# Performance work log

Hardware: AMD Instinct MI355X
Metric: run time of the kernel (lower is better)

## Reference

```python
import jax, jax.numpy as jnp
import numpy as np

HIDDEN = 1024
HEADS = 16
HEAD_DIM = HIDDEN // HEADS  # 64
BLOCK = 1024  # block_size; seq_len > BLOCK triggers ring path
B, S = 1, 4096


def setup_inputs() -> dict:
    key = jax.random.key(0)
    k0, k1, k2, k3, k4 = jax.random.split(key, 5)
    w_scale = 0.02
    return {
        "hidden_states": jax.random.normal(k0, (B, S, HIDDEN), dtype=jnp.float32),
        # weights stored [in, out]; applied as x @ W (equivalent to nn.Linear with W.T)
        "w_q": jax.random.normal(k1, (HIDDEN, HIDDEN), dtype=jnp.float32) * w_scale,
        "w_k": jax.random.normal(k2, (HIDDEN, HIDDEN), dtype=jnp.float32) * w_scale,
        "w_v": jax.random.normal(k3, (HIDDEN, HIDDEN), dtype=jnp.float32) * w_scale,
        "w_o": jax.random.normal(k4, (HIDDEN, HIDDEN), dtype=jnp.float32) * w_scale,
    }


def _ring_attention(q, k, v, block, scale):
    # q,k,v: [B, H, S, D]. Faithful to the torch module: each KV block subtracts
    # its OWN local max (no running-max rescale); exp-sums and weighted-V are
    # accumulated additively across KV blocks, then normalized once at the end.
    b, h, s, d = q.shape
    nb = s // block
    kb = jnp.moveaxis(k.reshape(b, h, nb, block, d), 2, 0)  # [nb, B, H, block, D]
    vb = jnp.moveaxis(v.reshape(b, h, nb, block, d), 2, 0)

    def step(carry, kv):
        num, den = carry
        k_blk, v_blk = kv
        s_blk = jnp.einsum("bhqd,bhkd->bhqk", q, k_blk) * scale  # [B,H,S,block]
        m = jnp.max(s_blk, axis=-1, keepdims=True)               # local max only
        e = jnp.exp(s_blk - m)
        num = num + jnp.einsum("bhqk,bhkd->bhqd", e, v_blk)
        den = den + jnp.sum(e, axis=-1, keepdims=True)
        return (num, den), None

    init = (jnp.zeros_like(q), jnp.zeros((b, h, s, 1), dtype=q.dtype))
    (num, den), _ = jax.lax.scan(step, init, (kb, vb))
    return num / den


def reference(hidden_states, w_q, w_k, w_v, w_o):
    b, s, _ = hidden_states.shape
    q = (hidden_states @ w_q).reshape(b, s, HEADS, HEAD_DIM).transpose(0, 2, 1, 3)
    k = (hidden_states @ w_k).reshape(b, s, HEADS, HEAD_DIM).transpose(0, 2, 1, 3)
    v = (hidden_states @ w_v).reshape(b, s, HEADS, HEAD_DIM).transpose(0, 2, 1, 3)
    scale = HEAD_DIM ** -0.5
    out = _ring_attention(q, k, v, BLOCK, scale)          # [B,H,S,D]
    out = out.transpose(0, 2, 1, 3).reshape(b, s, HIDDEN)  # [B,S,hidden]
    return out @ w_o
```

## Files before the change

kernel.cpp:

```cpp
#include <hip/hip_runtime.h>
#include <hip/hip_bf16.h>

typedef __bf16 bf16;
typedef bf16 bf16x2 __attribute__((ext_vector_type(2)));
typedef bf16 bf16x4 __attribute__((ext_vector_type(4)));
typedef bf16 bf16x8 __attribute__((ext_vector_type(8)));
typedef float f32x4 __attribute__((ext_vector_type(4)));

#define HID 1024
#define NHEADS 16
#define HD 64
#define SEQ 4096

__device__ __forceinline__ void gll16(const void* g, void* l) {
  __builtin_amdgcn_global_load_lds(
      (const __attribute__((address_space(1))) void*)g,
      (__attribute__((address_space(3))) void*)l, 16, 0, 0);
}

__device__ __forceinline__ float fast_exp2(float x) {
#if __has_builtin(__builtin_amdgcn_exp2f)
  return __builtin_amdgcn_exp2f(x);
#else
  return __expf(x * 0.6931471805599453f);
#endif
}

__global__ __launch_bounds__(256)
void prep_kernel(const float* __restrict__ X,
                 const float* __restrict__ Wq, const float* __restrict__ Wk,
                 const float* __restrict__ Wv, const float* __restrict__ Wo,
                 bf16* __restrict__ Xb, bf16* __restrict__ Wt)
{
  const int z = blockIdx.z, t = threadIdx.x, bx = blockIdx.x;
  if (z == 0) {
    const float4* src = (const float4*)X;
    const int gid = bx * 256 + t;
    #pragma unroll
    for (int i = 0; i < 16; ++i) {
      float4 v = src[gid + i * 65536];
      bf16x4 o = {(bf16)v.x, (bf16)v.y, (bf16)v.z, (bf16)v.w};
      *(bf16x4*)&Xb[(size_t)(gid + i * 65536) * 4] = o;
    }
  } else {
    const float* W = (z == 1) ? Wq : (z == 2) ? Wk : (z == 3) ? Wv : Wo;
    bf16* dst = Wt + (size_t)(z - 1) * HID * HID;
    const float scale = (z == 1) ? 0.18033688011112042f : 1.0f;
    __shared__ bf16 T[64][68];
    const int tr = (bx >> 4) * 64, tc = (bx & 15) * 64;
    #pragma unroll
    for (int p = 0; p < 4; ++p) {
      int row = (t >> 4) + p * 16;
      float4 v = *(const float4*)&W[(size_t)(tr + row) * HID + tc + (t & 15) * 4];
      T[row][(t & 15) * 4 + 0] = (bf16)(v.x * scale);
      T[row][(t & 15) * 4 + 1] = (bf16)(v.y * scale);
      T[row][(t & 15) * 4 + 2] = (bf16)(v.z * scale);
      T[row][(t & 15) * 4 + 3] = (bf16)(v.w * scale);
    }
    __syncthreads();
    #pragma unroll
    for (int p = 0; p < 4; ++p) {
      int rp = (t >> 4) + p * 16;
      int cb = (t & 15) * 4;
      bf16x4 o = {T[cb + 0][rp], T[cb + 1][rp], T[cb + 2][rp], T[cb + 3][rp]};
      *(bf16x4*)&dst[(size_t)(tc + rp) * HID + tr + cb] = o;
    }
  }
}

__global__ __launch_bounds__(256)
void qkv_gemm(const bf16* __restrict__ A, const bf16* __restrict__ Wt,
              bf16* __restrict__ Qg, bf16* __restrict__ Kg,
              bf16* __restrict__ Vt)
{
  __shared__ bf16 sbuf[16384];
  bf16* As = sbuf;
  bf16* Bs = sbuf + 8192;

  const int t = threadIdx.x, lane = t & 63, w = t >> 6;
  const int z = blockIdx.z;
  const int n0 = blockIdx.x * 128, m0 = blockIdx.y * 128;
  const bf16* Bt = Wt + (size_t)z * HID * HID;
  const int wm = (w & 1) * 64, wn = (w >> 1) * 64;
  const int fr = lane & 15, quad = lane >> 4;

  f32x4 acc[4][4] = {};

  const int sr = lane >> 3;
  const int sc = ((lane & 7) - sr) & 7;
  const bf16* ga = A  + (size_t)(m0 + w * 32 + sr) * HID + sc * 8;
  const bf16* gb = Bt + (size_t)(n0 + w * 32 + sr) * HID + sc * 8;

  for (int k0 = 0; k0 < HID; k0 += 64) {
    __syncthreads();
    #pragma unroll
    for (int c = 0; c < 4; ++c) {
      gll16(ga + (size_t)(c * 8) * HID + k0, As + (w * 32 + c * 8) * 64);
      gll16(gb + (size_t)(c * 8) * HID + k0, Bs + (w * 32 + c * 8) * 64);
    }
    __syncthreads();
    #pragma unroll
    for (int ks = 0; ks < 2; ++ks) {
      bf16x8 af[4], bg[4];
      #pragma unroll
      for (int i = 0; i < 4; ++i)
        af[i] = *(const bf16x8*)&As[(wm + i * 16 + fr) * 64 +
                                    ((ks * 4 + quad + fr) & 7) * 8];
      #pragma unroll
      for (int i = 0; i < 4; ++i)
        bg[i] = *(const bf16x8*)&Bs[(wn + i * 16 + fr) * 64 +
                                    ((ks * 4 + quad + fr) & 7) * 8];
      #pragma unroll
      for (int mi = 0; mi < 4; ++mi)
        #pragma unroll
        for (int ni = 0; ni < 4; ++ni)
          acc[mi][ni] = __builtin_amdgcn_mfma_f32_16x16x32_bf16(
              af[mi], bg[ni], acc[mi][ni], 0, 0, 0);
    }
  }

  if (z < 2) {
    bf16* C = z ? Kg : Qg;
    #pragma unroll
    for (int mi = 0; mi < 4; ++mi)
      #pragma unroll
      for (int ni = 0; ni < 4; ++ni)
        #pragma unroll
        for (int r = 0; r < 4; ++r)
          C[(size_t)(m0 + wm + mi * 16 + quad * 4 + r) * HID +
            n0 + wn + ni * 16 + fr] = (bf16)acc[mi][ni][r];
  } else {
    __syncthreads();
    #pragma unroll
    for (int mi = 0; mi < 4; ++mi)
      #pragma unroll
      for (int ni = 0; ni < 4; ++ni)
        #pragma unroll
        for (int r = 0; r < 4; ++r) {
          int row = wn + ni * 16 + fr;
          int col = wm + mi * 16 + quad * 4 + r;
          int colS = (col + 8 * (row & 15)) & 127;
          sbuf[row * 128 + colS] = (bf16)acc[mi][ni][r];
        }
    __syncthreads();
    const int row = t >> 1, cb = (t & 1) * 64;
    #pragma unroll
    for (int j = 0; j < 8; ++j) {
      int c0 = (cb + j * 8 + 8 * (row & 15)) & 127;
      *(bf16x8*)&Vt[(size_t)(n0 + row) * SEQ + m0 + cb + j * 8] =
          *(const bf16x8*)&sbuf[row * 128 + c0];
    }
  }
}

__global__ __launch_bounds__(256)
void oproj_gemm(const bf16* __restrict__ A, const bf16* __restrict__ Bt,
                float* __restrict__ C)
{
  __shared__ bf16 sbuf[16384];
  bf16* As = sbuf;
  bf16* Bs = sbuf + 8192;

  const int t = threadIdx.x, lane = t & 63, w = t >> 6;
  const int n0 = blockIdx.x * 128, m0 = blockIdx.y * 128;
  const int wm = (w & 1) * 64, wn = (w >> 1) * 64;
  const int fr = lane & 15, quad = lane >> 4;

  f32x4 acc[4][4] = {};

  const int sr = lane >> 3;
  const int sc = ((lane & 7) - sr) & 7;
  const bf16* ga = A  + (size_t)(m0 + w * 32 + sr) * HID + sc * 8;
  const bf16* gb = Bt + (size_t)(n0 + w * 32 + sr) * HID + sc * 8;

  for (int k0 = 0; k0 < HID; k0 += 64) {
    __syncthreads();
    #pragma unroll
    for (int c = 0; c < 4; ++c) {
      gll16(ga + (size_t)(c * 8) * HID + k0, As + (w * 32 + c * 8) * 64);
      gll16(gb + (size_t)(c * 8) * HID + k0, Bs + (w * 32 + c * 8) * 64);
    }
    __syncthreads();
    #pragma unroll
    for (int ks = 0; ks < 2; ++ks) {
      bf16x8 af[4], bg[4];
      #pragma unroll
      for (int i = 0; i < 4; ++i)
        af[i] = *(const bf16x8*)&As[(wm + i * 16 + fr) * 64 +
                                    ((ks * 4 + quad + fr) & 7) * 8];
      #pragma unroll
      for (int i = 0; i < 4; ++i)
        bg[i] = *(const bf16x8*)&Bs[(wn + i * 16 + fr) * 64 +
                                    ((ks * 4 + quad + fr) & 7) * 8];
      #pragma unroll
      for (int mi = 0; mi < 4; ++mi)
        #pragma unroll
        for (int ni = 0; ni < 4; ++ni)
          acc[mi][ni] = __builtin_amdgcn_mfma_f32_16x16x32_bf16(
              af[mi], bg[ni], acc[mi][ni], 0, 0, 0);
    }
  }

  #pragma unroll
  for (int mi = 0; mi < 4; ++mi)
    #pragma unroll
    for (int ni = 0; ni < 4; ++ni)
      #pragma unroll
      for (int r = 0; r < 4; ++r)
        C[(size_t)(m0 + wm + mi * 16 + quad * 4 + r) * HID +
          n0 + wn + ni * 16 + fr] = acc[mi][ni][r];
}

#define THR_L2 12.0f

__global__ __launch_bounds__(256, 2)
void attn5(const bf16* __restrict__ Q, const bf16* __restrict__ K,
           const bf16* __restrict__ Vt, bf16* __restrict__ O)
{
  __shared__ bf16 Ks[2][4096];
  __shared__ bf16 Vs[2][4096];
  __shared__ bf16 Ps[4][1024];

  const int t = threadIdx.x, lane = t & 63, w = t >> 6;
  const int h = blockIdx.y, q0 = blockIdx.x * 128;
  const int fr = lane & 15, quad = lane >> 4;

  bf16x8 bq[2][2];
  #pragma unroll
  for (int qf = 0; qf < 2; ++qf)
    #pragma unroll
    for (int ks = 0; ks < 2; ++ks)
      bq[qf][ks] = *(const bf16x8*)&Q[(size_t)(q0 + w * 32 + qf * 16 + fr) * HID
                                      + h * 64 + ks * 32 + quad * 8];

  const int sr = lane >> 3;
  const int sc = ((lane & 7) - sr) & 7;
  const bf16* gk = K  + (size_t)(w * 16 + sr) * HID + h * 64 + sc * 8;
  const bf16* gv = Vt + (size_t)(h * 64 + w * 16 + sr) * SEQ + sc * 8;

  #pragma unroll
  for (int j = 0; j < 2; ++j) {
    gll16(gk + (size_t)(j * 8) * HID, &Ks[0][(w * 16 + j * 8) * 64]);
    gll16(gv + (size_t)(j * 8) * SEQ, &Vs[0][(w * 16 + j * 8) * 64]);
  }

  f32x4 accN[2][4] = {};
  f32x4 accO[2][4] = {};
  float m_used[2] = {-3e38f, -3e38f}, m_true[2] = {-3e38f, -3e38f};
  float l_i[2] = {0.f, 0.f}, den[2] = {0.f, 0.f};

  __syncthreads();

  for (int kk = 0; kk < 64; ++kk) {
    const int buf = kk & 1;
    if (kk < 63) {
      const size_t key0n = (size_t)(kk + 1) * 64;
      #pragma unroll
      for (int j = 0; j < 2; ++j) {
        gll16(gk + (key0n + j * 8) * HID, &Ks[buf ^ 1][(w * 16 + j * 8) * 64]);
        gll16(gv + key0n + (size_t)(j * 8) * SEQ,
              &Vs[buf ^ 1][(w * 16 + j * 8) * 64]);
      }
    }

    bf16x8 ak[4][2];
    #pragma unroll
    for (int mt = 0; mt < 4; ++mt)
      #pragma unroll
      for (int ks = 0; ks < 2; ++ks)
        ak[mt][ks] = *(const bf16x8*)&Ks[buf][(mt * 16 + fr) * 64 +
                                             ((ks * 4 + quad + fr) & 7) * 8];

    f32x4 s[2][4];
    #pragma unroll
    for (int qf = 0; qf < 2; ++qf)
      #pragma unroll
      for (int mt = 0; mt < 4; ++mt) {
        f32x4 z = {};
        z = __builtin_amdgcn_mfma_f32_16x16x32_bf16(ak[mt][0], bq[qf][0], z, 0, 0, 0);
        z = __builtin_amdgcn_mfma_f32_16x16x32_bf16(ak[mt][1], bq[qf][1], z, 0, 0, 0);
        s[qf][mt] = z;
      }

    bf16x8 bp[2][2];
    #pragma unroll
    for (int qf = 0; qf < 2; ++qf) {
      float mx0 = fmaxf(fmaxf(s[qf][0][0], s[qf][0][1]), fmaxf(s[qf][0][2], s[qf][0][3]));
      float mx1 = fmaxf(fmaxf(s[qf][1][0], s[qf][1][1]), fmaxf(s[qf][1][2], s[qf][1][3]));
      float mx2 = fmaxf(fmaxf(s[qf][2][0], s[qf][2][1]), fmaxf(s[qf][2][2], s[qf][2][3]));
      float mx3 = fmaxf(fmaxf(s[qf][3][0], s[qf][3][1]), fmaxf(s[qf][3][2], s[qf][3][3]));
      float mx = fmaxf(fmaxf(mx0, mx1), fmaxf(mx2, mx3));
      mx = fmaxf(mx, __shfl_xor(mx, 16));
      mx = fmaxf(mx, __shfl_xor(mx, 32));
      m_true[qf] = fmaxf(m_true[qf], mx);

      if (__any(mx > m_used[qf] + THR_L2)) {
        const float mn = fmaxf(m_used[qf], mx);
        const float a = fast_exp2(m_used[qf] - mn);
        m_used[qf] = mn;
        l_i[qf] *= a;
        #pragma unroll
        for (int dt = 0; dt < 4; ++dt) accO[qf][dt] *= a;
      }

      float sum = 0.f;
      const int prow = fr * 64;
      #pragma unroll
      for (int mt = 0; mt < 4; ++mt) {
        float p0 = fast_exp2(s[qf][mt][0] - m_used[qf]);
        float p1 = fast_exp2(s[qf][mt][1] - m_used[qf]);
        float p2 = fast_exp2(s[qf][mt][2] - m_used[qf]);
        float p3 = fast_exp2(s[qf][mt][3] - m_used[qf]);
        sum += (p0 + p1) + (p2 + p3);
        bf16x4 pv = {(bf16)p0, (bf16)p1, (bf16)p2, (bf16)p3};
        *(bf16x4*)&Ps[w][prow + ((mt * 2 + (quad >> 1) + fr) & 7) * 8 +
                         (quad & 1) * 4] = pv;
      }
      sum += __shfl_xor(sum, 16);
      sum += __shfl_xor(sum, 32);
      l_i[qf] += sum;

      #pragma unroll
      for (int ks = 0; ks < 2; ++ks)
        bp[qf][ks] = *(const bf16x8*)&Ps[w][fr * 64 +
                                            ((ks * 4 + quad + fr) & 7) * 8];
    }

    #pragma unroll
    for (int ks = 0; ks < 2; ++ks)
      #pragma unroll
      for (int dt = 0; dt < 4; ++dt) {
        bf16x8 av = *(const bf16x8*)&Vs[buf][(dt * 16 + fr) * 64 +
                                            ((ks * 4 + quad + fr) & 7) * 8];
        accO[0][dt] = __builtin_amdgcn_mfma_f32_16x16x32_bf16(av, bp[0][ks], accO[0][dt], 0, 0, 0);
        accO[1][dt] = __builtin_amdgcn_mfma_f32_16x16x32_bf16(av, bp[1][ks], accO[1][dt], 0, 0, 0);
      }

    if ((kk & 15) == 15) {
      #pragma unroll
      for (int qf = 0; qf < 2; ++qf) {
        const float c = fast_exp2(m_used[qf] - m_true[qf]);
        den[qf] += l_i[qf] * c;
        #pragma unroll
        for (int dt = 0; dt < 4; ++dt)
          #pragma unroll
          for (int r = 0; r < 4; ++r) accN[qf][dt][r] += accO[qf][dt][r] * c;
        #pragma unroll
        for (int dt = 0; dt < 4; ++dt) accO[qf][dt] = (f32x4){0.f, 0.f, 0.f, 0.f};
        l_i[qf] = 0.f; m_used[qf] = -3e38f; m_true[qf] = -3e38f;
      }
    }
    __syncthreads();
  }

  #pragma unroll
  for (int qf = 0; qf < 2; ++qf) {
    const float inv = 1.0f / den[qf];
    const size_t orow = (size_t)(q0 + w * 32 + qf * 16 + fr) * HID + h * 64;
    #pragma unroll
    for (int dt = 0; dt < 4; ++dt) {
      bf16x4 ov = {(bf16)(accN[qf][dt][0] * inv), (bf16)(accN[qf][dt][1] * inv),
                   (bf16)(accN[qf][dt][2] * inv), (bf16)(accN[qf][dt][3] * inv)};
      *(bf16x4*)&O[orow + dt * 16 + quad * 4] = ov;
    }
  }
}

extern "C" void kernel_launch(void* const* d_in, const int* in_sizes, int n_in,
                              void* d_out, int out_size, void* d_ws, size_t ws_size,
                              hipStream_t stream)
{
  const float* X  = (const float*)d_in[0];
  const float* Wq = (const float*)d_in[1];
  const float* Wk = (const float*)d_in[2];
  const float* Wv = (const float*)d_in[3];
  const float* Wo = (const float*)d_in[4];
  float* out = (float*)d_out;

  const size_t MB = 1024 * 1024;
  bf16* Xb  = (bf16*)d_ws;
  bf16* Wt  = (bf16*)((char*)d_ws + 8  * MB);
  bf16* Qg  = (bf16*)((char*)d_ws + 16 * MB);
  bf16* Kg  = (bf16*)((char*)d_ws + 24 * MB);
  bf16* Vtg = (bf16*)((char*)d_ws + 32 * MB);
  bf16* Og  = (bf16*)((char*)d_ws + 40 * MB);

  prep_kernel<<<dim3(256, 1, 5), 256, 0, stream>>>(X, Wq, Wk, Wv, Wo, Xb, Wt);
  qkv_gemm<<<dim3(HID / 128, SEQ / 128, 3), 256, 0, stream>>>(Xb, Wt, Qg, Kg, Vtg);
  attn5<<<dim3(SEQ / 128, NHEADS), 256, 0, stream>>>(Qg, Kg, Vtg, Og);
  oproj_gemm<<<dim3(HID / 128, SEQ / 128), 256, 0, stream>>>(
      Og, Wt + (size_t)3 * HID * HID, out);
}
```

Baseline: 263.2 us.

## Split attention KV range across two blocks and combine partials in separate kernel

The attention kernel now splits the KV sequence into two halves along a new grid dimension, doubling the block count from 512 to 1024, and raises occupancy hints to 4 blocks per CU. Each half writes unnormalized fp32 numerators and denominators to workspace, and a new combine kernel sums them and normalizes into bf16. This targets under-filled CUs on the attention pass. The cost is an extra kernel launch and about 32 MB of fp32 partial traffic, and the fallback path is taken only if the workspace is too small.

```diff
diff --git a/kernel.cpp b/kernel.cpp
--- a/kernel.cpp
+++ b/kernel.cpp
@@ -213,16 +213,17 @@
 
 #define THR_L2 12.0f
 
-__global__ __launch_bounds__(256, 2)
-void attn5(const bf16* __restrict__ Q, const bf16* __restrict__ K,
-           const bf16* __restrict__ Vt, bf16* __restrict__ O)
+__global__ __launch_bounds__(256, 4)
+void attn6(const bf16* __restrict__ Q, const bf16* __restrict__ K,
+           const bf16* __restrict__ Vt, float* __restrict__ Num,
+           float* __restrict__ Den)
 {
   __shared__ bf16 Ks[2][4096];
   __shared__ bf16 Vs[2][4096];
   __shared__ bf16 Ps[4][1024];
 
   const int t = threadIdx.x, lane = t & 63, w = t >> 6;
-  const int h = blockIdx.y, q0 = blockIdx.x * 128;
+  const int h = blockIdx.y, q0 = blockIdx.x * 128, half = blockIdx.z;
   const int fr = lane & 15, quad = lane >> 4;
 
   bf16x8 bq[2][2];
@@ -235,8 +236,8 @@
 
   const int sr = lane >> 3;
   const int sc = ((lane & 7) - sr) & 7;
-  const bf16* gk = K  + (size_t)(w * 16 + sr) * HID + h * 64 + sc * 8;
-  const bf16* gv = Vt + (size_t)(h * 64 + w * 16 + sr) * SEQ + sc * 8;
+  const bf16* gk = K  + (size_t)(half * 2048 + w * 16 + sr) * HID + h * 64 + sc * 8;
+  const bf16* gv = Vt + (size_t)(h * 64 + w * 16 + sr) * SEQ + half * 2048 + sc * 8;
 
   #pragma unroll
   for (int j = 0; j < 2; ++j) {
@@ -251,9 +252,9 @@
 
   __syncthreads();
 
-  for (int kk = 0; kk < 64; ++kk) {
+  for (int kk = 0; kk < 32; ++kk) {
     const int buf = kk & 1;
-    if (kk < 63) {
+    if (kk < 31) {
       const size_t key0n = (size_t)(kk + 1) * 64;
       #pragma unroll
       for (int j = 0; j < 2; ++j) {
@@ -353,6 +354,176 @@
     __syncthreads();
   }
 
+  float* numH = Num + (size_t)half * SEQ * HID;
+  #pragma unroll
+  for (int qf = 0; qf < 2; ++qf) {
+    const int qrow = q0 + w * 32 + qf * 16 + fr;
+    const size_t orow = (size_t)qrow * HID + h * 64;
+    #pragma unroll
+    for (int dt = 0; dt < 4; ++dt)
+      *(f32x4*)&numH[orow + dt * 16 + quad * 4] = accN[qf][dt];
+    if (quad == 0)
+      Den[((size_t)half * 16 + h) * SEQ + qrow] = den[qf];
+  }
+}
+
+__global__ __launch_bounds__(256)
+void combine_kernel(const float* __restrict__ Num, const float* __restrict__ Den,
+                    bf16* __restrict__ Og)
+{
+  const int gid = blockIdx.x * 256 + threadIdx.x;
+  const int idx = gid * 4;
+  const int row = idx >> 10, col = idx & 1023, h = col >> 6;
+  const float d0 = Den[(size_t)h * SEQ + row];
+  const float d1 = Den[((size_t)16 + h) * SEQ + row];
+  const float inv = 1.0f / (d0 + d1);
+  f32x4 a = *(const f32x4*)&Num[idx];
+  f32x4 b = *(const f32x4*)&Num[(size_t)SEQ * HID + idx];
+  bf16x4 o = {(bf16)((a[0] + b[0]) * inv), (bf16)((a[1] + b[1]) * inv),
+              (bf16)((a[2] + b[2]) * inv), (bf16)((a[3] + b[3]) * inv)};
+  *(bf16x4*)&Og[idx] = o;
+}
+
+__global__ __launch_bounds__(256, 2)
+void attn5(const bf16* __restrict__ Q, const bf16* __restrict__ K,
+           const bf16* __restrict__ Vt, bf16* __restrict__ O)
+{
+  __shared__ bf16 Ks[2][4096];
+  __shared__ bf16 Vs[2][4096];
+  __shared__ bf16 Ps[4][1024];
+
+  const int t = threadIdx.x, lane = t & 63, w = t >> 6;
+  const int h = blockIdx.y, q0 = blockIdx.x * 128;
+  const int fr = lane & 15, quad = lane >> 4;
+
+  bf16x8 bq[2][2];
+  #pragma unroll
+  for (int qf = 0; qf < 2; ++qf)
+    #pragma unroll
+    for (int ks = 0; ks < 2; ++ks)
+      bq[qf][ks] = *(const bf16x8*)&Q[(size_t)(q0 + w * 32 + qf * 16 + fr) * HID
+                                      + h * 64 + ks * 32 + quad * 8];
+
+  const int sr = lane >> 3;
+  const int sc = ((lane & 7) - sr) & 7;
+  const bf16* gk = K  + (size_t)(w * 16 + sr) * HID + h * 64 + sc * 8;
+  const bf16* gv = Vt + (size_t)(h * 64 + w * 16 + sr) * SEQ + sc * 8;
+
+  #pragma unroll
+  for (int j = 0; j < 2; ++j) {
+    gll16(gk + (size_t)(j * 8) * HID, &Ks[0][(w * 16 + j * 8) * 64]);
+    gll16(gv + (size_t)(j * 8) * SEQ, &Vs[0][(w * 16 + j * 8) * 64]);
+  }
+
+  f32x4 accN[2][4] = {};
+  f32x4 accO[2][4] = {};
+  float m_used[2] = {-3e38f, -3e38f}, m_true[2] = {-3e38f, -3e38f};
+  float l_i[2] = {0.f, 0.f}, den[2] = {0.f, 0.f};
+
+  __syncthreads();
+
+  for (int kk = 0; kk < 64; ++kk) {
+    const int buf = kk & 1;
+    if (kk < 63) {
+      const size_t key0n = (size_t)(kk + 1) * 64;
+      #pragma unroll
+      for (int j = 0; j < 2; ++j) {
+        gll16(gk + (key0n + j * 8) * HID, &Ks[buf ^ 1][(w * 16 + j * 8) * 64]);
+        gll16(gv + key0n + (size_t)(j * 8) * SEQ,
+              &Vs[buf ^ 1][(w * 16 + j * 8) * 64]);
+      }
+    }
+
+    bf16x8 ak[4][2];
+    #pragma unroll
+    for (int mt = 0; mt < 4; ++mt)
+      #pragma unroll
+      for (int ks = 0; ks < 2; ++ks)
+        ak[mt][ks] = *(const bf16x8*)&Ks[buf][(mt * 16 + fr) * 64 +
+                                             ((ks * 4 + quad + fr) & 7) * 8];
+
+    f32x4 s[2][4];
+    #pragma unroll
+    for (int qf = 0; qf < 2; ++qf)
+      #pragma unroll
+      for (int mt = 0; mt < 4; ++mt) {
+        f32x4 z = {};
+        z = __builtin_amdgcn_mfma_f32_16x16x32_bf16(ak[mt][0], bq[qf][0], z, 0, 0, 0);
+        z = __builtin_amdgcn_mfma_f32_16x16x32_bf16(ak[mt][1], bq[qf][1], z, 0, 0, 0);
+        s[qf][mt] = z;
+      }
+
+    bf16x8 bp[2][2];
+    #pragma unroll
+    for (int qf = 0; qf < 2; ++qf) {
+      float mx0 = fmaxf(fmaxf(s[qf][0][0], s[qf][0][1]), fmaxf(s[qf][0][2], s[qf][0][3]));
+      float mx1 = fmaxf(fmaxf(s[qf][1][0], s[qf][1][1]), fmaxf(s[qf][1][2], s[qf][1][3]));
+      float mx2 = fmaxf(fmaxf(s[qf][2][0], s[qf][2][1]), fmaxf(s[qf][2][2], s[qf][2][3]));
+      float mx3 = fmaxf(fmaxf(s[qf][3][0], s[qf][3][1]), fmaxf(s[qf][3][2], s[qf][3][3]));
+      float mx = fmaxf(fmaxf(mx0, mx1), fmaxf(mx2, mx3));
+      mx = fmaxf(mx, __shfl_xor(mx, 16));
+      mx = fmaxf(mx, __shfl_xor(mx, 32));
+      m_true[qf] = fmaxf(m_true[qf], mx);
+
+      if (__any(mx > m_used[qf] + THR_L2)) {
+        const float mn = fmaxf(m_used[qf], mx);
+        const float a = fast_exp2(m_used[qf] - mn);
+        m_used[qf] = mn;
+        l_i[qf] *= a;
+        #pragma unroll
+        for (int dt = 0; dt < 4; ++dt) accO[qf][dt] *= a;
+      }
+
+      float sum = 0.f;
+      const int prow = fr * 64;
+      #pragma unroll
+      for (int mt = 0; mt < 4; ++mt) {
+        float p0 = fast_exp2(s[qf][mt][0] - m_used[qf]);
+        float p1 = fast_exp2(s[qf][mt][1] - m_used[qf]);
+        float p2 = fast_exp2(s[qf][mt][2] - m_used[qf]);
+        float p3 = fast_exp2(s[qf][mt][3] - m_used[qf]);
+        sum += (p0 + p1) + (p2 + p3);
+        bf16x4 pv = {(bf16)p0, (bf16)p1, (bf16)p2, (bf16)p3};
+        *(bf16x4*)&Ps[w][prow + ((mt * 2 + (quad >> 1) + fr) & 7) * 8 +
+                         (quad & 1) * 4] = pv;
+      }
+      sum += __shfl_xor(sum, 16);
+      sum += __shfl_xor(sum, 32);
+      l_i[qf] += sum;
+
+      #pragma unroll
+      for (int ks = 0; ks < 2; ++ks)
+        bp[qf][ks] = *(const bf16x8*)&Ps[w][fr * 64 +
+                                            ((ks * 4 + quad + fr) & 7) * 8];
+    }
+
+    #pragma unroll
+    for (int ks = 0; ks < 2; ++ks)
+      #pragma unroll
+      for (int dt = 0; dt < 4; ++dt) {
+        bf16x8 av = *(const bf16x8*)&Vs[buf][(dt * 16 + fr) * 64 +
+                                            ((ks * 4 + quad + fr) & 7) * 8];
+        accO[0][dt] = __builtin_amdgcn_mfma_f32_16x16x32_bf16(av, bp[0][ks], accO[0][dt], 0, 0, 0);
+        accO[1][dt] = __builtin_amdgcn_mfma_f32_16x16x32_bf16(av, bp[1][ks], accO[1][dt], 0, 0, 0);
+      }
+
+    if ((kk & 15) == 15) {
+      #pragma unroll
+      for (int qf = 0; qf < 2; ++qf) {
+        const float c = fast_exp2(m_used[qf] - m_true[qf]);
+        den[qf] += l_i[qf] * c;
+        #pragma unroll
+        for (int dt = 0; dt < 4; ++dt)
+          #pragma unroll
+          for (int r = 0; r < 4; ++r) accN[qf][dt][r] += accO[qf][dt][r] * c;
+        #pragma unroll
+        for (int dt = 0; dt < 4; ++dt) accO[qf][dt] = (f32x4){0.f, 0.f, 0.f, 0.f};
+        l_i[qf] = 0.f; m_used[qf] = -3e38f; m_true[qf] = -3e38f;
+      }
+    }
+    __syncthreads();
+  }
+
   #pragma unroll
   for (int qf = 0; qf < 2; ++qf) {
     const float inv = 1.0f / den[qf];
@@ -378,16 +549,23 @@
   float* out = (float*)d_out;
 
   const size_t MB = 1024 * 1024;
-  bf16* Xb  = (bf16*)d_ws;
-  bf16* Wt  = (bf16*)((char*)d_ws + 8  * MB);
-  bf16* Qg  = (bf16*)((char*)d_ws + 16 * MB);
-  bf16* Kg  = (bf16*)((char*)d_ws + 24 * MB);
-  bf16* Vtg = (bf16*)((char*)d_ws + 32 * MB);
-  bf16* Og  = (bf16*)((char*)d_ws + 40 * MB);
+  bf16*  Xb  = (bf16*)d_ws;
+  bf16*  Wt  = (bf16*)((char*)d_ws + 8  * MB);
+  bf16*  Qg  = (bf16*)((char*)d_ws + 16 * MB);
+  bf16*  Kg  = (bf16*)((char*)d_ws + 24 * MB);
+  bf16*  Vtg = (bf16*)((char*)d_ws + 32 * MB);
+  bf16*  Og  = (bf16*)((char*)d_ws + 40 * MB);
+  float* Num = (float*)((char*)d_ws + 48 * MB);
+  float* Den = (float*)((char*)d_ws + 80 * MB);
 
   prep_kernel<<<dim3(256, 1, 5), 256, 0, stream>>>(X, Wq, Wk, Wv, Wo, Xb, Wt);
   qkv_gemm<<<dim3(HID / 128, SEQ / 128, 3), 256, 0, stream>>>(Xb, Wt, Qg, Kg, Vtg);
-  attn5<<<dim3(SEQ / 128, NHEADS), 256, 0, stream>>>(Qg, Kg, Vtg, Og);
+  if (ws_size >= 81 * MB) {
+    attn6<<<dim3(SEQ / 128, NHEADS, 2), 256, 0, stream>>>(Qg, Kg, Vtg, Num, Den);
+    combine_kernel<<<dim3(SEQ * HID / 1024, 1, 1), 256, 0, stream>>>(Num, Den, Og);
+  } else {
+    attn5<<<dim3(SEQ / 128, NHEADS), 256, 0, stream>>>(Qg, Kg, Vtg, Og);
+  }
   oproj_gemm<<<dim3(HID / 128, SEQ / 128), 256, 0, stream>>>(
       Og, Wt + (size_t)3 * HID * HID, out);
 }
```

New measurement: 268.3 us. Within noise of the previous version (+2.0%).

## Split attention KV range across two blocks with 32x32 MFMA and combine kernel

Applied to the files above, without the earlier changes.

Adds attn8, which splits the 4096-key range into two halves via blockIdx.z, doubling the grid and raising occupancy to 4 blocks per CU. Each 32-query wave computes S with 32x32x16 MFMAs and keeps P in registers via cross-lane shuffles, removing the LDS staging of P. It writes normalized per-ring-block partial outputs plus adjusted denominators for each 1024-key block. A new combine8 kernel reweights and sums them into Og. This costs an extra launch and partial-output traffic, and it runs only when the workspace holds at least 81 MB.

```diff
diff --git a/kernel.cpp b/kernel.cpp
--- a/kernel.cpp
+++ b/kernel.cpp
@@ -6,6 +6,8 @@
 typedef bf16 bf16x4 __attribute__((ext_vector_type(4)));
 typedef bf16 bf16x8 __attribute__((ext_vector_type(8)));
 typedef float f32x4 __attribute__((ext_vector_type(4)));
+typedef float f32x16 __attribute__((ext_vector_type(16)));
+typedef unsigned int u32x4 __attribute__((ext_vector_type(4)));
 
 #define HID 1024
 #define NHEADS 16
@@ -212,6 +214,187 @@
 }
 
 #define THR_L2 12.0f
+
+__global__ __launch_bounds__(256, 4)
+void attn8(const bf16* __restrict__ Q, const bf16* __restrict__ K,
+           const bf16* __restrict__ Vt, bf16* __restrict__ Opart,
+           float* __restrict__ Den)
+{
+  __shared__ bf16 Ks[2][4096];
+  __shared__ bf16 Vs[2][4096];
+
+  const int t = threadIdx.x, lane = t & 63, w = t >> 6;
+  const int h = blockIdx.y, q0 = blockIdx.x * 128, half = blockIdx.z;
+  const int q = lane & 31, hi = lane >> 5;
+  const int qrow = q0 + w * 32 + q;
+
+  bf16x8 bq[4];
+  #pragma unroll
+  for (int j = 0; j < 4; ++j)
+    bq[j] = *(const bf16x8*)&Q[(size_t)qrow * HID + h * 64 + j * 16 + hi * 8];
+
+  const int sr = lane >> 3;
+  const int sc = ((lane & 7) - sr) & 7;
+  const bf16* gk = K  + (size_t)(half * 2048 + w * 16 + sr) * HID + h * 64 + sc * 8;
+  const bf16* gv = Vt + (size_t)(h * 64 + w * 16 + sr) * SEQ + half * 2048 + sc * 8;
+
+  #pragma unroll
+  for (int j = 0; j < 2; ++j) {
+    gll16(gk + (size_t)(j * 8) * HID, &Ks[0][(w * 16 + j * 8) * 64]);
+    gll16(gv + (size_t)(j * 8) * SEQ, &Vs[0][(w * 16 + j * 8) * 64]);
+  }
+
+  f32x16 accO[2];
+  #pragma unroll
+  for (int r = 0; r < 16; ++r) { accO[0][r] = 0.f; accO[1][r] = 0.f; }
+  float m_used = -3e38f, m_true = -3e38f, l_i = 0.f;
+
+  __syncthreads();
+
+  for (int kk = 0; kk < 32; ++kk) {
+    const int buf = kk & 1;
+    if (kk < 31) {
+      const size_t key0n = (size_t)(kk + 1) * 64;
+      #pragma unroll
+      for (int j = 0; j < 2; ++j) {
+        gll16(gk + (key0n + j * 8) * HID, &Ks[buf ^ 1][(w * 16 + j * 8) * 64]);
+        gll16(gv + key0n + (size_t)(j * 8) * SEQ,
+              &Vs[buf ^ 1][(w * 16 + j * 8) * 64]);
+      }
+    }
+
+    #pragma unroll
+    for (int st = 0; st < 2; ++st) {
+      const int r0 = st * 32;
+      f32x16 s;
+      #pragma unroll
+      for (int r = 0; r < 16; ++r) s[r] = 0.f;
+      #pragma unroll
+      for (int j = 0; j < 4; ++j) {
+        const int row = r0 + q;
+        bf16x8 ak = *(const bf16x8*)&Ks[buf][row * 64 +
+                                            ((j * 2 + hi + row) & 7) * 8];
+        s = __builtin_amdgcn_mfma_f32_32x32x16_bf16(ak, bq[j], s, 0, 0, 0);
+      }
+
+      float mx = s[0];
+      #pragma unroll
+      for (int r = 1; r < 16; ++r) mx = fmaxf(mx, s[r]);
+      mx = fmaxf(mx, __shfl_xor(mx, 32));
+      m_true = fmaxf(m_true, mx);
+
+      if (__any(mx > m_used + THR_L2)) {
+        const float mn = fmaxf(m_used, mx);
+        const float a = fast_exp2(m_used - mn);
+        m_used = mn; l_i *= a;
+        #pragma unroll
+        for (int r = 0; r < 16; ++r) { accO[0][r] *= a; accO[1][r] *= a; }
+      }
+
+      float p[16], sum = 0.f;
+      #pragma unroll
+      for (int r = 0; r < 16; ++r) { p[r] = fast_exp2(s[r] - m_used); sum += p[r]; }
+      sum += __shfl_xor(sum, 32);
+      l_i += sum;
+
+      unsigned pk[8];
+      #pragma unroll
+      for (int i = 0; i < 8; ++i) {
+        bf16x2 pp = {(bf16)p[2 * i], (bf16)p[2 * i + 1]};
+        pk[i] = __builtin_bit_cast(unsigned, pp);
+      }
+      unsigned e0 = __shfl_xor(hi ? pk[0] : pk[2], 32);
+      unsigned e1 = __shfl_xor(hi ? pk[1] : pk[3], 32);
+      unsigned e2 = __shfl_xor(hi ? pk[4] : pk[6], 32);
+      unsigned e3 = __shfl_xor(hi ? pk[5] : pk[7], 32);
+      u32x4 w0 = {hi ? e0 : pk[0], hi ? e1 : pk[1],
+                  hi ? pk[2] : e0, hi ? pk[3] : e1};
+      u32x4 w1 = {hi ? e2 : pk[4], hi ? e3 : pk[5],
+                  hi ? pk[6] : e2, hi ? pk[7] : e3};
+      bf16x8 bp0 = __builtin_bit_cast(bf16x8, w0);
+      bf16x8 bp1 = __builtin_bit_cast(bf16x8, w1);
+
+      #pragma unroll
+      for (int db = 0; db < 2; ++db) {
+        const int rowd = db * 32 + q;
+        bf16x8 av0 = *(const bf16x8*)&Vs[buf][rowd * 64 +
+                       ((st * 4 + 0 + hi + rowd) & 7) * 8];
+        accO[db] = __builtin_amdgcn_mfma_f32_32x32x16_bf16(av0, bp0, accO[db], 0, 0, 0);
+        bf16x8 av1 = *(const bf16x8*)&Vs[buf][rowd * 64 +
+                       ((st * 4 + 2 + hi + rowd) & 7) * 8];
+        accO[db] = __builtin_amdgcn_mfma_f32_32x32x16_bf16(av1, bp1, accO[db], 0, 0, 0);
+      }
+    }
+
+    if ((kk & 15) == 15) {
+      const int rb = half * 2 + (kk >> 4);
+      const float inv = 1.0f / l_i;
+      const size_t base =
+          ((size_t)(rb * 16 + h) * 128 + (q0 >> 5) + w) * 2048 + (size_t)lane * 32;
+      #pragma unroll
+      for (int j = 0; j < 4; ++j) {
+        bf16x8 wv;
+        #pragma unroll
+        for (int e = 0; e < 8; ++e)
+          wv[e] = (bf16)(accO[j >> 1][(j & 1) * 8 + e] * inv);
+        *(bf16x8*)&Opart[base + j * 8] = wv;
+      }
+      if (hi == 0)
+        Den[(size_t)(rb * 16 + h) * SEQ + qrow] =
+            l_i * fast_exp2(m_used - m_true);
+      #pragma unroll
+      for (int r = 0; r < 16; ++r) { accO[0][r] = 0.f; accO[1][r] = 0.f; }
+      l_i = 0.f; m_used = -3e38f; m_true = -3e38f;
+    }
+    __syncthreads();
+  }
+}
+
+__global__ __launch_bounds__(64)
+void combine8(const bf16* __restrict__ Opart, const float* __restrict__ Den,
+              bf16* __restrict__ Og)
+{
+  __shared__ bf16 T[32][72];
+  const int lane = threadIdx.x & 63;
+  const int h = blockIdx.y, qs = blockIdx.x;
+  const int q = lane & 31, hi = lane >> 5;
+
+  float dw[4];
+  #pragma unroll
+  for (int rb = 0; rb < 4; ++rb)
+    dw[rb] = Den[(size_t)(rb * 16 + h) * SEQ + qs * 32 + q];
+  const float inv = 1.0f / (dw[0] + dw[1] + dw[2] + dw[3]);
+
+  float acc[32];
+  #pragma unroll
+  for (int i = 0; i < 32; ++i) acc[i] = 0.f;
+  #pragma unroll
+  for (int rb = 0; rb < 4; ++rb) {
+    const float wq = dw[rb] * inv;
+    const size_t base =
+        ((size_t)(rb * 16 + h) * 128 + qs) * 2048 + (size_t)lane * 32;
+    #pragma unroll
+    for (int j = 0; j < 4; ++j) {
+      bf16x8 v = *(const bf16x8*)&Opart[base + j * 8];
+      #pragma unroll
+      for (int e = 0; e < 8; ++e) acc[j * 8 + e] += wq * (float)v[e];
+    }
+  }
+
+  #pragma unroll
+  for (int idx = 0; idx < 32; ++idx) {
+    const int db = idx >> 4, r = idx & 15;
+    const int d = db * 32 + (r & 3) + 8 * (r >> 2) + 4 * hi;
+    T[q][d] = (bf16)acc[idx];
+  }
+  __syncthreads();
+  #pragma unroll
+  for (int p = 0; p < 4; ++p) {
+    const int row = p * 8 + (lane >> 3);
+    *(bf16x8*)&Og[(size_t)(qs * 32 + row) * HID + h * 64 + (lane & 7) * 8] =
+        *(const bf16x8*)&T[row][(lane & 7) * 8];
+  }
+}
 
 __global__ __launch_bounds__(256, 2)
 void attn5(const bf16* __restrict__ Q, const bf16* __restrict__ K,
@@ -378,16 +561,23 @@
   float* out = (float*)d_out;
 
   const size_t MB = 1024 * 1024;
-  bf16* Xb  = (bf16*)d_ws;
-  bf16* Wt  = (bf16*)((char*)d_ws + 8  * MB);
-  bf16* Qg  = (bf16*)((char*)d_ws + 16 * MB);
-  bf16* Kg  = (bf16*)((char*)d_ws + 24 * MB);
-  bf16* Vtg = (bf16*)((char*)d_ws + 32 * MB);
-  bf16* Og  = (bf16*)((char*)d_ws + 40 * MB);
+  bf16*  Xb  = (bf16*)d_ws;
+  bf16*  Wt  = (bf16*)((char*)d_ws + 8  * MB);
+  bf16*  Qg  = (bf16*)((char*)d_ws + 16 * MB);
+  bf16*  Kg  = (bf16*)((char*)d_ws + 24 * MB);
+  bf16*  Vtg = (bf16*)((char*)d_ws + 32 * MB);
+  bf16*  Og  = (bf16*)((char*)d_ws + 40 * MB);
+  bf16*  Opart = (bf16*)((char*)d_ws + 48 * MB);
+  float* Den   = (float*)((char*)d_ws + 80 * MB);
 
   prep_kernel<<<dim3(256, 1, 5), 256, 0, stream>>>(X, Wq, Wk, Wv, Wo, Xb, Wt);
   qkv_gemm<<<dim3(HID / 128, SEQ / 128, 3), 256, 0, stream>>>(Xb, Wt, Qg, Kg, Vtg);
-  attn5<<<dim3(SEQ / 128, NHEADS), 256, 0, stream>>>(Qg, Kg, Vtg, Og);
+  if (ws_size >= 81 * MB) {
+    attn8<<<dim3(SEQ / 128, NHEADS, 2), 256, 0, stream>>>(Qg, Kg, Vtg, Opart, Den);
+    combine8<<<dim3(SEQ / 32, NHEADS), 64, 0, stream>>>(Opart, Den, Og);
+  } else {
+    attn5<<<dim3(SEQ / 128, NHEADS), 256, 0, stream>>>(Qg, Kg, Vtg, Og);
+  }
   oproj_gemm<<<dim3(HID / 128, SEQ / 128), 256, 0, stream>>>(
       Og, Wt + (size_t)3 * HID * HID, out);
 }
```

After: 254.2 us. -3.4%, faster.
